# Kernel tuning notes

Measured on AMD Instinct MI355X. Metric: run time of the kernel, lower is better.

The kernel has to match this reference:

```python
import jax, jax.numpy as jnp
import numpy as np

N_NODES = 100000
N_EDGES = 1600000
IN_CH = 64
HIDDEN = 64
OUT_DIM = HIDDEN // 2  # 32


def setup_inputs() -> dict:
    key = jax.random.key(0)
    ks = jax.random.split(key, 10)
    x = jax.random.normal(ks[0], (N_NODES, IN_CH), dtype=jnp.float32)
    edge_index = jax.random.randint(ks[1], (2, N_EDGES), 0, N_NODES, dtype=jnp.int64)
    s = 1.0 / np.sqrt(IN_CH)
    sh = 1.0 / np.sqrt(HIDDEN)
    # SAGEConv layer 1: lin_l (with bias) on aggregated neighbors, lin_r (no bias) on root
    w1l = jax.random.uniform(ks[2], (HIDDEN, IN_CH), jnp.float32, -s, s)
    b1 = jax.random.uniform(ks[3], (HIDDEN,), jnp.float32, -s, s)
    w1r = jax.random.uniform(ks[4], (HIDDEN, IN_CH), jnp.float32, -s, s)
    # SAGEConv layer 2
    w2l = jax.random.uniform(ks[5], (HIDDEN, HIDDEN), jnp.float32, -sh, sh)
    b2 = jax.random.uniform(ks[6], (HIDDEN,), jnp.float32, -sh, sh)
    w2r = jax.random.uniform(ks[7], (HIDDEN, HIDDEN), jnp.float32, -sh, sh)
    # readout head
    wh = jax.random.uniform(ks[8], (OUT_DIM, HIDDEN), jnp.float32, -sh, sh)
    bh = jax.random.uniform(ks[9], (OUT_DIM,), jnp.float32, -sh, sh)
    return {"x": x, "edge_index": edge_index, "w1l": w1l, "b1": b1, "w1r": w1r,
            "w2l": w2l, "b2": b2, "w2r": w2r, "wh": wh, "bh": bh}


def _sage_conv(h, src, dst, wl, bl, wr):
    # mean-aggregate messages from src nodes onto dst nodes
    msg = h[src]                                            # [E, d]
    agg = jax.ops.segment_sum(msg, dst, num_segments=N_NODES)  # [N, d]
    deg = jax.ops.segment_sum(jnp.ones((msg.shape[0],), h.dtype), dst,
                              num_segments=N_NODES)            # [N]
    mean = agg / jnp.maximum(deg, 1.0)[:, None]
    return mean @ wl.T + bl + h @ wr.T


def reference(x, edge_index, w1l, b1, w1r, w2l, b2, w2r, wh, bh):
    src, dst = edge_index[0], edge_index[1]
    # dropout layers are identity in eval mode
    h = jax.nn.relu(_sage_conv(x, src, dst, w1l, b1, w1r))
    h = jax.nn.relu(_sage_conv(h, src, dst, w2l, b2, w2r))
    return h @ wh.T + bh
```

## Files before the change

### kernel.cpp

```cpp
#include <hip/hip_runtime.h>


#define D 64
#define OUTD 32
#define REG_SHIFT 8
#define REG_SIZE 256
#define BCHUNK 4096
#define PADQ 16
#define CAP 5120
#define OUTCAP 8960

#define OFF_FLAG     0
#define OFF_RCUR     64
#define OFF_DEG      576
#define OFF_ROWSTART 100928
#define OFF_INV      201280
#define OFF_COL      301632
#define OFF_EBUF     3804992
#define OFF_XB       5806912
#define OFF_H1B      9006944
#define OFF_MEANB    12206976
#define OFF_WC1      15406976
#define OFF_WC2      15411072
#define OFF_WHB      15415168

typedef __attribute__((ext_vector_type(8))) short bf16x8;
typedef __attribute__((ext_vector_type(4))) float f32x4;
typedef __attribute__((ext_vector_type(2))) float f32x2;

__device__ __forceinline__ unsigned short bf16rne(float x) {
    unsigned u = __float_as_uint(x);
    unsigned r = (u + 0x7FFFu + ((u >> 16) & 1u)) >> 16;
    return (unsigned short)r;
}

__global__ void detect_init(const int* __restrict__ e32, int* __restrict__ flag,
                            int* __restrict__ rcur, int NR) {
    int t = threadIdx.x;
    if (t < 64) {
        int v = e32[2 * t + 1];
        unsigned long long m = __ballot(v != 0);
        if (t == 0) flag[0] = (m == 0ULL) ? 1 : 0;
    }
    if (t < NR) rcur[t] = t * CAP;
}

__global__ __launch_bounds__(256) void bin_prep(
        const int* __restrict__ e32, const int* __restrict__ flag,
        int* __restrict__ rcur, int* __restrict__ ebuf, int E, int NR, int bblocks,
        const float* __restrict__ x, unsigned short* __restrict__ xb,
        unsigned short* __restrict__ h1b,
        const float* __restrict__ w1l, const float* __restrict__ w1r,
        const float* __restrict__ w2l, const float* __restrict__ w2r,
        const float* __restrict__ wh,
        unsigned short* __restrict__ wcat1, unsigned short* __restrict__ wcat2,
        unsigned short* __restrict__ whb, int n4, int N) {
    __shared__ int stage[BCHUNK];
    __shared__ unsigned short rgn[BCHUNK];
    __shared__ int hist[512], lbase[512], startr[512], s1[512];
    int t = threadIdx.x;

    if (blockIdx.x >= bblocks) {
        int i = (blockIdx.x - bblocks) * 256 + t;
        if (i < n4) {
            float4 v = ((const float4*)x)[i];
            unsigned lo = (unsigned)bf16rne(v.x) | ((unsigned)bf16rne(v.y) << 16);
            unsigned hi = (unsigned)bf16rne(v.z) | ((unsigned)bf16rne(v.w) << 16);
            ((uint2*)xb)[i] = make_uint2(lo, hi);
            return;
        }
        int j = i - n4;
        if (j < 16) {
            ((uint2*)xb)[(size_t)N * 16 + j] = make_uint2(0u, 0u);
        } else if (j < 32) {
            ((uint2*)h1b)[(size_t)N * 16 + (j - 16)] = make_uint2(0u, 0u);
        } else if (j < 32 + 8192) {
            int q = j - 32;
            int o = q >> 7, k = q & 127;
            wcat1[q] = bf16rne(k < 64 ? w1l[o * 64 + k] : w1r[o * 64 + k - 64]);
        } else if (j < 32 + 16384) {
            int q = j - 32 - 8192;
            int o = q >> 7, k = q & 127;
            wcat2[q] = bf16rne(k < 64 ? w2l[o * 64 + k] : w2r[o * 64 + k - 64]);
        } else if (j < 32 + 16384 + 2048) {
            int q = j - 32 - 16384;
            whb[q] = bf16rne(wh[q]);
        }
        return;
    }

    int mode = flag[0];
    int base = blockIdx.x * BCHUNK;
    for (int i = t; i < 512; i += 256) hist[i] = 0;
    __syncthreads();
    for (int j = t; j < BCHUNK; j += 256) {
        int i = base + j;
        if (i < E) {
            int d = mode ? e32[2 * (E + i)] : e32[E + i];
            atomicAdd(&hist[d >> REG_SHIFT], 1);
        }
    }
    __syncthreads();
    {
        int* a = lbase; int* b = s1;
        for (int i = t; i < 512; i += 256) a[i] = hist[i];
        __syncthreads();
        for (int off = 1; off < 512; off <<= 1) {
            for (int i = t; i < 512; i += 256)
                b[i] = a[i] + ((i >= off) ? a[i - off] : 0);
            __syncthreads();
            int* tmp = a; a = b; b = tmp;
        }
        for (int i = t; i < 512; i += 256) {
            int incl = a[i];
            int ex = incl - hist[i];
            __syncthreads();
            lbase[i] = ex;
        }
        __syncthreads();
    }
    for (int i = t; i < 512; i += 256) {
        int st = 0;
        if (i < NR && hist[i] > 0) {
            st = atomicAdd(&rcur[i], hist[i]);
            int lim = (i + 1) * CAP - hist[i];
            if (st > lim) st = lim;
        }
        startr[i] = st;
    }
    __syncthreads();
    for (int i = t; i < 512; i += 256) hist[i] = 0;
    __syncthreads();
    for (int j = t; j < BCHUNK; j += 256) {
        int i = base + j;
        if (i < E) {
            int s = mode ? e32[2 * i]       : e32[i];
            int d = mode ? e32[2 * (E + i)] : e32[E + i];
            int r = d >> REG_SHIFT;
            int o = atomicAdd(&hist[r], 1);
            int pos = lbase[r] + o;
            stage[pos] = ((d & (REG_SIZE - 1)) << 24) | s;
            rgn[pos] = (unsigned short)r;
        }
    }
    __syncthreads();
    int count = E - base; if (count > BCHUNK) count = BCHUNK;
    for (int i = t; i < count; i += 256) {
        int r = rgn[i];
        ebuf[startr[r] + (i - lbase[r])] = stage[i];
    }
}

__global__ __launch_bounds__(256) void build_csr(
        const int* __restrict__ ebuf, const int* __restrict__ rcur,
        int* __restrict__ degP, int* __restrict__ rowStartP, float* __restrict__ inv,
        int* __restrict__ colP, int N) {
    __shared__ int hist[REG_SIZE], cur[REG_SIZE], sA[REG_SIZE], sB[REG_SIZE];
    int r = blockIdx.x;
    int t = threadIdx.x;
    int lo = r << REG_SHIFT;
    int e0 = r * CAP, e1 = rcur[r];
    int colPbase = r * OUTCAP;
    hist[t] = 0;
    __syncthreads();
    for (int i = e0 + t; i < e1; i += 256)
        atomicAdd(&hist[((unsigned)ebuf[i]) >> 24], 1);
    __syncthreads();
    int v = hist[t];
    int vp = (v + PADQ - 1) & ~(PADQ - 1);
    int* a = sA; int* b = sB;
    a[t] = vp;
    __syncthreads();
    for (int off = 1; off < 256; off <<= 1) {
        b[t] = a[t] + ((t >= off) ? a[t - off] : 0);
        __syncthreads();
        int* tmp = a; a = b; b = tmp;
    }
    int startP = colPbase + (a[t] - vp);
    int node = lo + t;
    if (node < N) {
        degP[node] = vp;
        rowStartP[node] = startP;
        inv[node] = 1.0f / (float)(v > 0 ? v : 1);
    }
    cur[t] = startP;
    __syncthreads();
    for (int i = e0 + t; i < e1; i += 256) {
        int p = ebuf[i];
        int pos = atomicAdd(&cur[((unsigned)p) >> 24], 1);
        colP[pos] = (p & 0xFFFFFF) << 7;
    }
    __syncthreads();
    int zoff = N << 7;
    for (int k = startP + v; k < startP + vp; ++k) colP[k] = zoff;
}

__global__ __launch_bounds__(256, 8) void gather_mean_bf16(
        const unsigned short* __restrict__ hb, const int* __restrict__ rowStartP,
        const int* __restrict__ degPv, const int* __restrict__ colP,
        const float* __restrict__ invdeg, unsigned short* __restrict__ meanb,
        int n) {
    int wid = (blockIdx.x * 256 + (int)threadIdx.x) >> 6;
    int lane = threadIdx.x & 63;
    if (wid >= n) return;
    int node = __builtin_amdgcn_readfirstlane(wid);

    int rs = rowStartP[node];
    int dgp = degPv[node];
    const char* hbC = (const char*)hb;
    int half = lane >> 5, l31 = lane & 31;
    unsigned voff = (unsigned)(l31 << 2);

    f32x2 a0 = {0.f, 0.f}, a1 = {0.f, 0.f}, a2 = {0.f, 0.f}, a3 = {0.f, 0.f};
    f32x2 a4 = {0.f, 0.f}, a5 = {0.f, 0.f}, a6 = {0.f, 0.f}, a7 = {0.f, 0.f};

    for (int base = 0; base < dgp; base += 64) {
        int cv = colP[rs + base + lane];
        int m = dgp - base; if (m > 64) m = 64;
        int pairs = m >> 1;
        int pb = half;
        for (int p = 0; p < pairs; p += 8) {
#define G(j, A) { \
            int cb = __shfl(cv, pb + 2 * (j)); \
            unsigned u = *(const unsigned*)(hbC + ((unsigned)cb + voff)); \
            f32x2 w = {__uint_as_float(u << 16), __uint_as_float(u & 0xFFFF0000u)}; \
            A += w; }
            G(0, a0)  G(1, a1)  G(2, a2)  G(3, a3)
            G(4, a4)  G(5, a5)  G(6, a6)  G(7, a7)
#undef G
            pb += 16;
        }
    }
    f32x2 s = ((a0 + a1) + (a2 + a3)) + ((a4 + a5) + (a6 + a7));
    float s0 = s.x + __shfl_xor(s.x, 32);
    float s1 = s.y + __shfl_xor(s.y, 32);
    float iv = invdeg[node];
    if (!half) {
        unsigned mo = (unsigned)bf16rne(s0 * iv) | ((unsigned)bf16rne(s1 * iv) << 16);
        ((unsigned*)meanb)[(size_t)node * 32 + l31] = mo;
    }
}

template <bool HEAD>
__global__ __launch_bounds__(256, 2) void dense_mfma(
        const unsigned short* __restrict__ meanb,
        const unsigned short* __restrict__ ownb,
        const unsigned short* __restrict__ wcat,
        const float* __restrict__ bias,
        unsigned short* __restrict__ houtb,
        const unsigned short* __restrict__ whb,
        const float* __restrict__ bh,
        float* __restrict__ outp,
        int n) {
    const int lane = threadIdx.x & 63;
    const int wave = threadIdx.x >> 6;
    const int l15 = lane & 15;
    const int kg  = lane >> 4;

    bf16x8 Bf[4][4];
#pragma unroll
    for (int nt = 0; nt < 4; ++nt)
#pragma unroll
        for (int s = 0; s < 4; ++s)
            Bf[nt][s] = *(const bf16x8*)(wcat + (nt * 16 + l15) * 128 + s * 32 + kg * 8);

    float biasc[4];
#pragma unroll
    for (int nt = 0; nt < 4; ++nt) biasc[nt] = bias[nt * 16 + l15];

    bf16x8 Hf[2][2];
    float bhc[2];
    if constexpr (HEAD) {
#pragma unroll
        for (int nt = 0; nt < 2; ++nt) {
#pragma unroll
            for (int s = 0; s < 2; ++s)
                Hf[nt][s] = *(const bf16x8*)(whb + (nt * 16 + l15) * 64 + s * 32 + kg * 8);
            bhc[nt] = bh[nt * 16 + l15];
        }
    }

    __shared__ unsigned short hlds[HEAD ? 4 * 16 * 64 : 64];

    const int ntiles = (n + 15) >> 4;
    const int stride = gridDim.x * 4;
    int tile = blockIdx.x * 4 + wave;
    if (tile >= ntiles) return;

    bf16x8 Ac[4], An[4];
    {
        int row = tile * 16 + l15; if (row >= n) row = n - 1;
        const unsigned short* mrow = meanb + (size_t)row * 64 + kg * 8;
        const unsigned short* orow = ownb  + (size_t)row * 64 + kg * 8;
        Ac[0] = *(const bf16x8*)(mrow);
        Ac[1] = *(const bf16x8*)(mrow + 32);
        Ac[2] = *(const bf16x8*)(orow);
        Ac[3] = *(const bf16x8*)(orow + 32);
    }

    while (true) {
        int nxt = tile + stride;
        bool hasNext = nxt < ntiles;
        if (hasNext) {
            int row = nxt * 16 + l15; if (row >= n) row = n - 1;
            const unsigned short* mrow = meanb + (size_t)row * 64 + kg * 8;
            const unsigned short* orow = ownb  + (size_t)row * 64 + kg * 8;
            An[0] = *(const bf16x8*)(mrow);
            An[1] = *(const bf16x8*)(mrow + 32);
            An[2] = *(const bf16x8*)(orow);
            An[3] = *(const bf16x8*)(orow + 32);
        }

        f32x4 acc[4];
#pragma unroll
        for (int nt = 0; nt < 4; ++nt) {
            f32x4 a = {biasc[nt], biasc[nt], biasc[nt], biasc[nt]};
            a = __builtin_amdgcn_mfma_f32_16x16x32_bf16(Ac[0], Bf[nt][0], a, 0, 0, 0);
            a = __builtin_amdgcn_mfma_f32_16x16x32_bf16(Ac[1], Bf[nt][1], a, 0, 0, 0);
            a = __builtin_amdgcn_mfma_f32_16x16x32_bf16(Ac[2], Bf[nt][2], a, 0, 0, 0);
            a = __builtin_amdgcn_mfma_f32_16x16x32_bf16(Ac[3], Bf[nt][3], a, 0, 0, 0);
            acc[nt] = a;
        }

        int nb = tile * 16;
        if constexpr (!HEAD) {
#pragma unroll
            for (int nt = 0; nt < 4; ++nt)
#pragma unroll
                for (int r = 0; r < 4; ++r) {
                    int row = nb + kg * 4 + r;
                    float h = fmaxf(acc[nt][r], 0.0f);
                    if (row < n) houtb[(size_t)row * 64 + nt * 16 + l15] = bf16rne(h);
                }
        } else {
            unsigned short* L = hlds + wave * 1024;
            int n7 = lane & 7;
#pragma unroll
            for (int nt = 0; nt < 4; ++nt) {
                int bGlob = nt * 2 + (l15 >> 3);
#pragma unroll
                for (int r = 0; r < 4; ++r) {
                    int m = kg * 4 + r;
                    float h = fmaxf(acc[nt][r], 0.0f);
                    L[m * 64 + ((bGlob ^ (m & 7)) * 8) + n7] = bf16rne(h);
                }
            }
            __builtin_amdgcn_wave_barrier();
            bf16x8 hA[2];
#pragma unroll
            for (int s = 0; s < 2; ++s) {
                int kb = s * 4 + kg;
                hA[s] = *(const bf16x8*)(L + l15 * 64 + ((kb ^ (l15 & 7)) * 8));
            }
            __builtin_amdgcn_wave_barrier();
            f32x4 acc2[2];
#pragma unroll
            for (int nt = 0; nt < 2; ++nt) {
                f32x4 a = {bhc[nt], bhc[nt], bhc[nt], bhc[nt]};
                a = __builtin_amdgcn_mfma_f32_16x16x32_bf16(hA[0], Hf[nt][0], a, 0, 0, 0);
                a = __builtin_amdgcn_mfma_f32_16x16x32_bf16(hA[1], Hf[nt][1], a, 0, 0, 0);
                acc2[nt] = a;
            }
#pragma unroll
            for (int nt = 0; nt < 2; ++nt)
#pragma unroll
                for (int r = 0; r < 4; ++r) {
                    int row = nb + kg * 4 + r;
                    if (row < n) outp[(size_t)row * 32 + nt * 16 + l15] = acc2[nt][r];
                }
        }

        if (!hasNext) break;
        tile = nxt;
#pragma unroll
        for (int q = 0; q < 4; ++q) Ac[q] = An[q];
    }
}

extern "C" void kernel_launch(void* const* d_in, const int* in_sizes, int n_in,
                              void* d_out, int out_size, void* d_ws, size_t ws_size,
                              hipStream_t stream) {
    const float* x   = (const float*)d_in[0];
    const int* edges = (const int*)d_in[1];
    const float* w1l = (const float*)d_in[2];
    const float* b1  = (const float*)d_in[3];
    const float* w1r = (const float*)d_in[4];
    const float* w2l = (const float*)d_in[5];
    const float* b2  = (const float*)d_in[6];
    const float* w2r = (const float*)d_in[7];
    const float* wh  = (const float*)d_in[8];
    const float* bh  = (const float*)d_in[9];
    float* out = (float*)d_out;

    const int N = in_sizes[0] / D;
    const int E = in_sizes[1] / 2;
    const int NR = (N + REG_SIZE - 1) >> REG_SHIFT;

    int* ws = (int*)d_ws;
    int*            flag     = ws + OFF_FLAG;
    int*            rcur     = ws + OFF_RCUR;
    int*            degP     = ws + OFF_DEG;
    int*            rowStartP= ws + OFF_ROWSTART;
    float*          inv      = (float*)(ws + OFF_INV);
    int*            colP     = ws + OFF_COL;
    int*            ebuf     = ws + OFF_EBUF;
    unsigned short* xb       = (unsigned short*)(ws + OFF_XB);
    unsigned short* h1b      = (unsigned short*)(ws + OFF_H1B);
    unsigned short* meanb    = (unsigned short*)(ws + OFF_MEANB);
    unsigned short* wcat1    = (unsigned short*)(ws + OFF_WC1);
    unsigned short* wcat2    = (unsigned short*)(ws + OFF_WC2);
    unsigned short* whb      = (unsigned short*)(ws + OFF_WHB);

    detect_init<<<1, 512, 0, stream>>>(edges, flag, rcur, NR);
    int bblocks = (E + BCHUNK - 1) / BCHUNK;
    int n4 = N * D / 4;
    int pblocks = (n4 + 32 + 16384 + 2048 + 255) / 256;
    bin_prep<<<bblocks + pblocks, 256, 0, stream>>>(
        edges, flag, rcur, ebuf, E, NR, bblocks,
        x, xb, h1b, w1l, w1r, w2l, w2r, wh, wcat1, wcat2, whb, n4, N);
    build_csr<<<NR, 256, 0, stream>>>(ebuf, rcur, degP, rowStartP, inv, colP, N);

    int gblocks = (N + 3) / 4;
    int ntiles = (N + 15) / 16;
    int dblocks = (ntiles + 7) / 8;

    gather_mean_bf16<<<gblocks, 256, 0, stream>>>(xb, rowStartP, degP, colP, inv,
                                                  meanb, N);
    dense_mfma<false><<<dblocks, 256, 0, stream>>>(meanb, xb, wcat1, b1,
                                                   h1b, nullptr, nullptr, nullptr, N);
    gather_mean_bf16<<<gblocks, 256, 0, stream>>>(h1b, rowStartP, degP, colP, inv,
                                                  meanb, N);
    dense_mfma<true><<<dblocks, 256, 0, stream>>>(meanb, h1b, wcat2, b2,
                                                  nullptr, whb, bh, out, N);
}
```

Measured before the change: 154.7 us.

## Fuse neighbor mean gather with dense MFMA layer into one kernel

Merges the gather-mean kernel and the dense MFMA kernel into a single per-layer kernel. Each 256-thread block gathers 16 nodes (4 per wave) into shared memory, then each wave computes one 16-column output tile with MFMA. This drops the meanb round trip through global memory and two kernel launches. In exchange, every block reloads the weights, and each wave waits at a block barrier for the slowest node's gather, which may cost load balance.

```diff
diff --git a/kernel.cpp b/kernel.cpp
--- a/kernel.cpp
+++ b/kernel.cpp
@@ -19,7 +19,6 @@
 #define OFF_EBUF     3804992
 #define OFF_XB       5806912
 #define OFF_H1B      9006944
-#define OFF_MEANB    12206976
 #define OFF_WC1      15406976
 #define OFF_WC2      15411072
 #define OFF_WHB      15415168
@@ -195,56 +194,11 @@
     for (int k = startP + v; k < startP + vp; ++k) colP[k] = zoff;
 }
 
-__global__ __launch_bounds__(256, 8) void gather_mean_bf16(
-        const unsigned short* __restrict__ hb, const int* __restrict__ rowStartP,
-        const int* __restrict__ degPv, const int* __restrict__ colP,
-        const float* __restrict__ invdeg, unsigned short* __restrict__ meanb,
-        int n) {
-    int wid = (blockIdx.x * 256 + (int)threadIdx.x) >> 6;
-    int lane = threadIdx.x & 63;
-    if (wid >= n) return;
-    int node = __builtin_amdgcn_readfirstlane(wid);
-
-    int rs = rowStartP[node];
-    int dgp = degPv[node];
-    const char* hbC = (const char*)hb;
-    int half = lane >> 5, l31 = lane & 31;
-    unsigned voff = (unsigned)(l31 << 2);
-
-    f32x2 a0 = {0.f, 0.f}, a1 = {0.f, 0.f}, a2 = {0.f, 0.f}, a3 = {0.f, 0.f};
-    f32x2 a4 = {0.f, 0.f}, a5 = {0.f, 0.f}, a6 = {0.f, 0.f}, a7 = {0.f, 0.f};
-
-    for (int base = 0; base < dgp; base += 64) {
-        int cv = colP[rs + base + lane];
-        int m = dgp - base; if (m > 64) m = 64;
-        int pairs = m >> 1;
-        int pb = half;
-        for (int p = 0; p < pairs; p += 8) {
-#define G(j, A) { \
-            int cb = __shfl(cv, pb + 2 * (j)); \
-            unsigned u = *(const unsigned*)(hbC + ((unsigned)cb + voff)); \
-            f32x2 w = {__uint_as_float(u << 16), __uint_as_float(u & 0xFFFF0000u)}; \
-            A += w; }
-            G(0, a0)  G(1, a1)  G(2, a2)  G(3, a3)
-            G(4, a4)  G(5, a5)  G(6, a6)  G(7, a7)
-#undef G
-            pb += 16;
-        }
-    }
-    f32x2 s = ((a0 + a1) + (a2 + a3)) + ((a4 + a5) + (a6 + a7));
-    float s0 = s.x + __shfl_xor(s.x, 32);
-    float s1 = s.y + __shfl_xor(s.y, 32);
-    float iv = invdeg[node];
-    if (!half) {
-        unsigned mo = (unsigned)bf16rne(s0 * iv) | ((unsigned)bf16rne(s1 * iv) << 16);
-        ((unsigned*)meanb)[(size_t)node * 32 + l31] = mo;
-    }
-}
-
 template <bool HEAD>
-__global__ __launch_bounds__(256, 2) void dense_mfma(
-        const unsigned short* __restrict__ meanb,
-        const unsigned short* __restrict__ ownb,
+__global__ __launch_bounds__(256, 8) void fused_layer(
+        const unsigned short* __restrict__ hb,
+        const int* __restrict__ rowStartP, const int* __restrict__ degPv,
+        const int* __restrict__ colP, const float* __restrict__ invdeg,
         const unsigned short* __restrict__ wcat,
         const float* __restrict__ bias,
         unsigned short* __restrict__ houtb,
@@ -252,128 +206,119 @@
         const float* __restrict__ bh,
         float* __restrict__ outp,
         int n) {
+    __shared__ unsigned meanT[16 * 32];
+    __shared__ unsigned short hT[HEAD ? 16 * 64 : 64];
+
     const int lane = threadIdx.x & 63;
-    const int wave = threadIdx.x >> 6;
-    const int l15 = lane & 15;
-    const int kg  = lane >> 4;
-
-    bf16x8 Bf[4][4];
-#pragma unroll
-    for (int nt = 0; nt < 4; ++nt)
-#pragma unroll
-        for (int s = 0; s < 4; ++s)
-            Bf[nt][s] = *(const bf16x8*)(wcat + (nt * 16 + l15) * 128 + s * 32 + kg * 8);
-
-    float biasc[4];
-#pragma unroll
-    for (int nt = 0; nt < 4; ++nt) biasc[nt] = bias[nt * 16 + l15];
-
-    bf16x8 Hf[2][2];
-    float bhc[2];
-    if constexpr (HEAD) {
-#pragma unroll
-        for (int nt = 0; nt < 2; ++nt) {
-#pragma unroll
-            for (int s = 0; s < 2; ++s)
-                Hf[nt][s] = *(const bf16x8*)(whb + (nt * 16 + l15) * 64 + s * 32 + kg * 8);
-            bhc[nt] = bh[nt * 16 + l15];
-        }
-    }
-
-    __shared__ unsigned short hlds[HEAD ? 4 * 16 * 64 : 64];
-
-    const int ntiles = (n + 15) >> 4;
-    const int stride = gridDim.x * 4;
-    int tile = blockIdx.x * 4 + wave;
-    if (tile >= ntiles) return;
-
-    bf16x8 Ac[4], An[4];
-    {
-        int row = tile * 16 + l15; if (row >= n) row = n - 1;
-        const unsigned short* mrow = meanb + (size_t)row * 64 + kg * 8;
-        const unsigned short* orow = ownb  + (size_t)row * 64 + kg * 8;
-        Ac[0] = *(const bf16x8*)(mrow);
-        Ac[1] = *(const bf16x8*)(mrow + 32);
-        Ac[2] = *(const bf16x8*)(orow);
-        Ac[3] = *(const bf16x8*)(orow + 32);
-    }
-
-    while (true) {
-        int nxt = tile + stride;
-        bool hasNext = nxt < ntiles;
-        if (hasNext) {
-            int row = nxt * 16 + l15; if (row >= n) row = n - 1;
-            const unsigned short* mrow = meanb + (size_t)row * 64 + kg * 8;
-            const unsigned short* orow = ownb  + (size_t)row * 64 + kg * 8;
-            An[0] = *(const bf16x8*)(mrow);
-            An[1] = *(const bf16x8*)(mrow + 32);
-            An[2] = *(const bf16x8*)(orow);
-            An[3] = *(const bf16x8*)(orow + 32);
-        }
-
-        f32x4 acc[4];
-#pragma unroll
-        for (int nt = 0; nt < 4; ++nt) {
-            f32x4 a = {biasc[nt], biasc[nt], biasc[nt], biasc[nt]};
-            a = __builtin_amdgcn_mfma_f32_16x16x32_bf16(Ac[0], Bf[nt][0], a, 0, 0, 0);
-            a = __builtin_amdgcn_mfma_f32_16x16x32_bf16(Ac[1], Bf[nt][1], a, 0, 0, 0);
-            a = __builtin_amdgcn_mfma_f32_16x16x32_bf16(Ac[2], Bf[nt][2], a, 0, 0, 0);
-            a = __builtin_amdgcn_mfma_f32_16x16x32_bf16(Ac[3], Bf[nt][3], a, 0, 0, 0);
-            acc[nt] = a;
-        }
-
-        int nb = tile * 16;
-        if constexpr (!HEAD) {
-#pragma unroll
-            for (int nt = 0; nt < 4; ++nt)
-#pragma unroll
-                for (int r = 0; r < 4; ++r) {
-                    int row = nb + kg * 4 + r;
-                    float h = fmaxf(acc[nt][r], 0.0f);
-                    if (row < n) houtb[(size_t)row * 64 + nt * 16 + l15] = bf16rne(h);
-                }
-        } else {
-            unsigned short* L = hlds + wave * 1024;
-            int n7 = lane & 7;
-#pragma unroll
-            for (int nt = 0; nt < 4; ++nt) {
-                int bGlob = nt * 2 + (l15 >> 3);
-#pragma unroll
-                for (int r = 0; r < 4; ++r) {
-                    int m = kg * 4 + r;
-                    float h = fmaxf(acc[nt][r], 0.0f);
-                    L[m * 64 + ((bGlob ^ (m & 7)) * 8) + n7] = bf16rne(h);
-                }
+    const int w    = threadIdx.x >> 6;
+    const int half = lane >> 5, l31 = lane & 31;
+    const int l15  = lane & 15, kg  = lane >> 4;
+    const char* hbC = (const char*)hb;
+    unsigned voff = (unsigned)(l31 << 2);
+
+    const int nb = blockIdx.x * 16;
+
+    for (int q = 0; q < 4; ++q) {
+        int node = nb + w * 4 + q;
+        int nodeC = node < n ? node : n - 1;
+        nodeC = __builtin_amdgcn_readfirstlane(nodeC);
+        int rs = rowStartP[nodeC];
+        int dgp = degPv[nodeC];
+
+        f32x2 a0 = {0.f, 0.f}, a1 = {0.f, 0.f}, a2 = {0.f, 0.f}, a3 = {0.f, 0.f};
+        f32x2 a4 = {0.f, 0.f}, a5 = {0.f, 0.f}, a6 = {0.f, 0.f}, a7 = {0.f, 0.f};
+
+        for (int base = 0; base < dgp; base += 64) {
+            int cv = colP[rs + base + lane];
+            int m = dgp - base; if (m > 64) m = 64;
+            int pairs = m >> 1;
+            int pb = half;
+            for (int p = 0; p < pairs; p += 8) {
+#define G(j, A) { \
+                int cb = __shfl(cv, pb + 2 * (j)); \
+                unsigned u = *(const unsigned*)(hbC + ((unsigned)cb + voff)); \
+                f32x2 ww = {__uint_as_float(u << 16), __uint_as_float(u & 0xFFFF0000u)}; \
+                A += ww; }
+                G(0, a0)  G(1, a1)  G(2, a2)  G(3, a3)
+                G(4, a4)  G(5, a5)  G(6, a6)  G(7, a7)
+#undef G
+                pb += 16;
             }
-            __builtin_amdgcn_wave_barrier();
+        }
+        f32x2 s = ((a0 + a1) + (a2 + a3)) + ((a4 + a5) + (a6 + a7));
+        float s0 = s.x + __shfl_xor(s.x, 32);
+        float s1 = s.y + __shfl_xor(s.y, 32);
+        float iv = invdeg[nodeC];
+        if (!half) {
+            int local = w * 4 + q;
+            unsigned mo = (unsigned)bf16rne(s0 * iv) | ((unsigned)bf16rne(s1 * iv) << 16);
+            int cb = l31 >> 2;
+            meanT[local * 32 + ((cb ^ (local & 7)) << 2) + (l31 & 3)] = mo;
+        }
+    }
+    __syncthreads();
+
+    const int nt = w;
+    bf16x8 Am[2];
+#pragma unroll
+    for (int s = 0; s < 2; ++s) {
+        int cb = s * 4 + kg;
+        Am[s] = *(const bf16x8*)&meanT[l15 * 32 + ((cb ^ (l15 & 7)) << 2)];
+    }
+    int arow = nb + l15; if (arow >= n) arow = n - 1;
+    const unsigned short* orow = hb + (size_t)arow * 64 + kg * 8;
+    bf16x8 Ao0 = *(const bf16x8*)(orow);
+    bf16x8 Ao1 = *(const bf16x8*)(orow + 32);
+    const unsigned short* wrow = wcat + (nt * 16 + l15) * 128 + kg * 8;
+    bf16x8 B0 = *(const bf16x8*)(wrow);
+    bf16x8 B1 = *(const bf16x8*)(wrow + 32);
+    bf16x8 B2 = *(const bf16x8*)(wrow + 64);
+    bf16x8 B3 = *(const bf16x8*)(wrow + 96);
+
+    float bc = bias[nt * 16 + l15];
+    f32x4 a = {bc, bc, bc, bc};
+    a = __builtin_amdgcn_mfma_f32_16x16x32_bf16(Am[0], B0, a, 0, 0, 0);
+    a = __builtin_amdgcn_mfma_f32_16x16x32_bf16(Am[1], B1, a, 0, 0, 0);
+    a = __builtin_amdgcn_mfma_f32_16x16x32_bf16(Ao0,  B2, a, 0, 0, 0);
+    a = __builtin_amdgcn_mfma_f32_16x16x32_bf16(Ao1,  B3, a, 0, 0, 0);
+
+    if constexpr (!HEAD) {
+#pragma unroll
+        for (int r = 0; r < 4; ++r) {
+            int rw = nb + kg * 4 + r;
+            float h = fmaxf(a[r], 0.0f);
+            if (rw < n) houtb[(size_t)rw * 64 + nt * 16 + l15] = bf16rne(h);
+        }
+    } else {
+        int bGlob = nt * 2 + (l15 >> 3);
+        int n7 = l15 & 7;
+#pragma unroll
+        for (int r = 0; r < 4; ++r) {
+            int m = kg * 4 + r;
+            float h = fmaxf(a[r], 0.0f);
+            hT[m * 64 + ((bGlob ^ (m & 7)) * 8) + n7] = bf16rne(h);
+        }
+        __syncthreads();
+        if (w < 2) {
             bf16x8 hA[2];
 #pragma unroll
             for (int s = 0; s < 2; ++s) {
                 int kb = s * 4 + kg;
-                hA[s] = *(const bf16x8*)(L + l15 * 64 + ((kb ^ (l15 & 7)) * 8));
+                hA[s] = *(const bf16x8*)(hT + l15 * 64 + ((kb ^ (l15 & 7)) * 8));
             }
-            __builtin_amdgcn_wave_barrier();
-            f32x4 acc2[2];
-#pragma unroll
-            for (int nt = 0; nt < 2; ++nt) {
-                f32x4 a = {bhc[nt], bhc[nt], bhc[nt], bhc[nt]};
-                a = __builtin_amdgcn_mfma_f32_16x16x32_bf16(hA[0], Hf[nt][0], a, 0, 0, 0);
-                a = __builtin_amdgcn_mfma_f32_16x16x32_bf16(hA[1], Hf[nt][1], a, 0, 0, 0);
-                acc2[nt] = a;
+            const unsigned short* hrow = whb + (w * 16 + l15) * 64 + kg * 8;
+            bf16x8 H0 = *(const bf16x8*)(hrow);
+            bf16x8 H1 = *(const bf16x8*)(hrow + 32);
+            float bc2 = bh[w * 16 + l15];
+            f32x4 a2 = {bc2, bc2, bc2, bc2};
+            a2 = __builtin_amdgcn_mfma_f32_16x16x32_bf16(hA[0], H0, a2, 0, 0, 0);
+            a2 = __builtin_amdgcn_mfma_f32_16x16x32_bf16(hA[1], H1, a2, 0, 0, 0);
+#pragma unroll
+            for (int r = 0; r < 4; ++r) {
+                int rw = nb + kg * 4 + r;
+                if (rw < n) outp[(size_t)rw * 32 + w * 16 + l15] = a2[r];
             }
-#pragma unroll
-            for (int nt = 0; nt < 2; ++nt)
-#pragma unroll
-                for (int r = 0; r < 4; ++r) {
-                    int row = nb + kg * 4 + r;
-                    if (row < n) outp[(size_t)row * 32 + nt * 16 + l15] = acc2[nt][r];
-                }
-        }
-
-        if (!hasNext) break;
-        tile = nxt;
-#pragma unroll
-        for (int q = 0; q < 4; ++q) Ac[q] = An[q];
+        }
     }
 }
 
@@ -406,7 +351,6 @@
     int*            ebuf     = ws + OFF_EBUF;
     unsigned short* xb       = (unsigned short*)(ws + OFF_XB);
     unsigned short* h1b      = (unsigned short*)(ws + OFF_H1B);
-    unsigned short* meanb    = (unsigned short*)(ws + OFF_MEANB);
     unsigned short* wcat1    = (unsigned short*)(ws + OFF_WC1);
     unsigned short* wcat2    = (unsigned short*)(ws + OFF_WC2);
     unsigned short* whb      = (unsigned short*)(ws + OFF_WHB);
@@ -420,16 +364,12 @@
         x, xb, h1b, w1l, w1r, w2l, w2r, wh, wcat1, wcat2, whb, n4, N);
     build_csr<<<NR, 256, 0, stream>>>(ebuf, rcur, degP, rowStartP, inv, colP, N);
 
-    int gblocks = (N + 3) / 4;
     int ntiles = (N + 15) / 16;
-    int dblocks = (ntiles + 7) / 8;
-
-    gather_mean_bf16<<<gblocks, 256, 0, stream>>>(xb, rowStartP, degP, colP, inv,
-                                                  meanb, N);
-    dense_mfma<false><<<dblocks, 256, 0, stream>>>(meanb, xb, wcat1, b1,
-                                                   h1b, nullptr, nullptr, nullptr, N);
-    gather_mean_bf16<<<gblocks, 256, 0, stream>>>(h1b, rowStartP, degP, colP, inv,
-                                                  meanb, N);
-    dense_mfma<true><<<dblocks, 256, 0, stream>>>(meanb, h1b, wcat2, b2,
-                                                  nullptr, whb, bh, out, N);
-}
+
+    fused_layer<false><<<ntiles, 256, 0, stream>>>(
+        xb, rowStartP, degP, colP, inv, wcat1, b1,
+        h1b, nullptr, nullptr, nullptr, N);
+    fused_layer<true><<<ntiles, 256, 0, stream>>>(
+        h1b, rowStartP, degP, colP, inv, wcat2, b2,
+        nullptr, whb, bh, out, N);
+}
```

After: 140.1 us. 9.4% less time.
